# Optimization experiments

Hardware: AMD Instinct MI355X
Metric: run time of the kernel (lower is better)

## Reference

```python
import jax, jax.numpy as jnp
import numpy as np

B, H, L, D = 8, 8, 2048, 512

def setup_inputs() -> dict:
    key = jax.random.key(0)
    k1, k2 = jax.random.split(key)
    x = jax.random.normal(k1, (B, H, L, D), dtype=jnp.float32)
    mask = jnp.ones((B, L), dtype=jnp.int32)  # unused by the layer's call()
    complex_weight = 0.02 * jax.random.normal(k2, (H, L, D, 2), dtype=jnp.float32)
    return {"x": x, "mask": mask, "complex_weight": complex_weight}

def reference(x, mask, complex_weight):
    # FFT over the innermost (model_size) axis, matching tf.signal.fft
    fft_x = jnp.fft.fft(x.astype(jnp.complex64), axis=-1)
    w = jax.lax.complex(complex_weight[..., 0], complex_weight[..., 1])  # (H, L, D)
    gated = w * fft_x  # broadcast over batch
    out = jnp.fft.ifft(gated, axis=-1).real.astype(jnp.float32)
    return out
```

## Files before the change

kernel.cpp:

```cpp
#include <hip/hip_runtime.h>
#include <math.h>


#define HL 16384

__device__ __forceinline__ float2 cadd(float2 a, float2 b){ return make_float2(a.x+b.x, a.y+b.y); }
__device__ __forceinline__ float2 csub(float2 a, float2 b){ return make_float2(a.x-b.x, a.y-b.y); }
__device__ __forceinline__ float2 cmul(float2 a, float2 b){ return make_float2(a.x*b.x - a.y*b.y, a.x*b.y + a.y*b.x); }

__device__ __forceinline__ float2 twiddle(float f) {
    return make_float2(__builtin_amdgcn_cosf(f), -__builtin_amdgcn_sinf(f));
}

__device__ __forceinline__ void lds_order() {
    __builtin_amdgcn_wave_barrier();
}

__device__ __forceinline__ void fft8(float2 x[8]) {
    const float c = 0.70710678118654752f;
    float2 u0 = cadd(x[0], x[4]);
    float2 u1 = cadd(x[1], x[5]);
    float2 u2 = cadd(x[2], x[6]);
    float2 u3 = cadd(x[3], x[7]);
    float2 v0 = csub(x[0], x[4]);
    float2 t1 = csub(x[1], x[5]);
    float2 t2 = csub(x[2], x[6]);
    float2 t3 = csub(x[3], x[7]);
    float2 v1 = make_float2(c*(t1.x + t1.y), c*(t1.y - t1.x));
    float2 v2 = make_float2(t2.y, -t2.x);
    float2 v3 = make_float2(c*(t3.y - t3.x), -c*(t3.x + t3.y));
    float2 p0 = cadd(u0, u2), p1 = cadd(u1, u3);
    float2 q0 = csub(u0, u2), q1t = csub(u1, u3);
    float2 q1 = make_float2(q1t.y, -q1t.x);
    x[0] = cadd(p0, p1);
    x[4] = csub(p0, p1);
    x[2] = cadd(q0, q1);
    x[6] = csub(q0, q1);
    float2 r0 = cadd(v0, v2), r1 = cadd(v1, v3);
    float2 s0 = csub(v0, v2), s1t = csub(v1, v3);
    float2 s1 = make_float2(s1t.y, -s1t.x);
    x[1] = cadd(r0, r1);
    x[5] = csub(r0, r1);
    x[3] = cadd(s0, s1);
    x[7] = csub(s0, s1);
}

__device__ __forceinline__ void fft512_t(float2 v[8], int role, int lane, float2* sc,
                                         const float2* __restrict__ twA,
                                         const float2 tw2[8])
{
    fft8(v);
    #pragma unroll
    for (int k = 1; k < 8; ++k) v[k] = cmul(v[k], twA[role*7 + (k-1)]);
    lds_order();
    #pragma unroll
    for (int k1 = 0; k1 < 8; ++k1) sc[k1*72 + role] = v[k1];
    lds_order();
    const int k1 = lane >> 3, m2 = lane & 7;
    float2 u[8];
    #pragma unroll
    for (int m1 = 0; m1 < 8; ++m1) u[m1] = sc[k1*72 + 8*m1 + m2];
    fft8(u);
    #pragma unroll
    for (int j = 1; j < 8; ++j) u[j] = cmul(u[j], tw2[j]);
    lds_order();
    #pragma unroll
    for (int j1 = 0; j1 < 8; ++j1) sc[k1*72 + 9*j1 + m2] = u[j1];
    lds_order();
    const int j1 = lane & 7;
    #pragma unroll
    for (int m = 0; m < 8; ++m) v[m] = sc[k1*72 + 9*j1 + m];
    fft8(v);
}

using gu32 = __attribute__((address_space(1))) const unsigned int;
using lu32 = __attribute__((address_space(3))) unsigned int;

__global__ __launch_bounds__(256, 4) void sgn_fft_vec(
    const float* __restrict__ x,
    const float* __restrict__ cw,
    float* __restrict__ out)
{
    __shared__ __align__(16) float2 sc[4][8*72];
    __shared__ __align__(16) float  cwb[4][1024];
    __shared__ __align__(16) float2 twA[64*7];

    const int tid  = threadIdx.x;
    const int wid  = tid >> 6;
    const int lane = tid & 63;
    const int dsl  = ((lane & 7) << 3) | (lane >> 3);
    const int hl   = blockIdx.x;

    const int r1 = (wid       * HL + hl) * 512;
    const int r2 = ((wid + 4) * HL + hl) * 512;

    {
        const float* cwrow = cw + (size_t)hl * 1024;
        #pragma unroll
        for (int c = 0; c < 4; ++c) {
            __builtin_amdgcn_global_load_lds((gu32*)(cwrow + c*256 + lane*4),
                                             (lu32*)(&cwb[wid][c*256]), 16, 0, 0);
        }
    }

    const float4 a0 = *(const float4*)(x + r1 + 4*lane);
    const float4 a1 = *(const float4*)(x + r1 + 4*lane + 256);
    const float4 b0 = *(const float4*)(x + r2 + 4*lane);
    const float4 b1 = *(const float4*)(x + r2 + 4*lane + 256);

    {
        const int role = tid & 63, j = tid >> 6;
        twA[role*7 + 2*j] = twiddle((float)(role*(2*j+1)) * (1.0f/512.0f));
        if (j < 3)
            twA[role*7 + 2*j + 1] = twiddle((float)(role*(2*j+2)) * (1.0f/512.0f));
    }
    float2 tw2[8];
    {
        const int m2 = lane & 7;
        tw2[1] = twiddle((float)m2 * (1.0f/64.0f));
        tw2[2] = cmul(tw2[1], tw2[1]);
        tw2[3] = cmul(tw2[1], tw2[2]);
        tw2[4] = cmul(tw2[2], tw2[2]);
        tw2[5] = cmul(tw2[1], tw2[4]);
        tw2[6] = cmul(tw2[2], tw2[4]);
        tw2[7] = cmul(tw2[3], tw2[4]);
    }
    __syncthreads();

    float2* scw = &sc[wid][0];

    {
        float2* AB = scw;
        *(float4*)&AB[      4*lane    ] = make_float4(a0.x, b0.x, a0.y, b0.y);
        *(float4*)&AB[      4*lane + 2] = make_float4(a0.z, b0.z, a0.w, b0.w);
        *(float4*)&AB[256 + 4*lane    ] = make_float4(a1.x, b1.x, a1.y, b1.y);
        *(float4*)&AB[256 + 4*lane + 2] = make_float4(a1.z, b1.z, a1.w, b1.w);
    }
    lds_order();
    float2 v[8];
    #pragma unroll
    for (int j = 0; j < 8; ++j) v[j] = scw[64*j + lane];
    lds_order();

    fft512_t(v, lane, lane, scw, twA, tw2);

    asm volatile("s_waitcnt vmcnt(0)" ::: "memory");
    {
        const float2* __restrict__ cwf = (const float2*)&cwb[wid][0];
        const float hs = 0.5f / 512.0f;
        #pragma unroll
        for (int j2 = 0; j2 < 8; ++j2) {
            const int k  = dsl + 64*j2;
            const int nk = (512 - k) & 511;
            const float2 wk  = cwf[k];
            const float2 wnk = cwf[nk];
            const float2 wp  = make_float2(hs*(wk.x + wnk.x), hs*(wk.y - wnk.y));
            const float2 g   = cmul(wp, v[j2]);
            v[j2] = make_float2(g.x, -g.y);
        }
    }

    fft512_t(v, dsl, lane, scw, twA, tw2);

    lds_order();
    {
        float2* OD = scw;
        #pragma unroll
        for (int j2 = 0; j2 < 8; ++j2)
            OD[dsl + 64*j2] = make_float2(v[j2].x, -v[j2].y);
    }
    lds_order();
    #pragma unroll
    for (int c = 0; c < 2; ++c) {
        const float2* OD = scw;
        const float4 p = *(const float4*)&OD[4*lane + 256*c];
        const float4 q = *(const float4*)&OD[4*lane + 256*c + 2];
        *(float4*)(out + r1 + 4*lane + 256*c) = make_float4(p.x, p.z, q.x, q.z);
        *(float4*)(out + r2 + 4*lane + 256*c) = make_float4(p.y, p.w, q.y, q.w);
    }
}

extern "C" void kernel_launch(void* const* d_in, const int* in_sizes, int n_in,
                              void* d_out, int out_size, void* d_ws, size_t ws_size,
                              hipStream_t stream) {
    const float* x  = (const float*)d_in[0];
    const float* cw = (const float*)d_in[2];
    float* out = (float*)d_out;

    sgn_fft_vec<<<dim3(HL), dim3(256), 0, stream>>>(x, cw, out);
}
```

Baseline: 473.8 us.

## Load x via global_load_lds, weights into registers, compute twiddles per thread

Inputs x are now DMA'd straight into LDS with global_load_lds, replacing register loads followed by an LDS interleave store. Weights are gathered directly from global memory into registers rather than staged in LDS. The shared twiddle table is dropped in favour of per-thread twiddle generation, which removes the block-wide __syncthreads. The aim is less LDS traffic and no block barrier, at the cost of uncoalesced float2 weight gathers (each weight element is fetched twice, once as wk and once as wnk) and extra ALU work for the twiddles.

```diff
diff --git a/kernel.cpp b/kernel.cpp
--- a/kernel.cpp
+++ b/kernel.cpp
@@ -45,13 +45,26 @@
     x[7] = csub(s0, s1);
 }
 
-__device__ __forceinline__ void fft512_t(float2 v[8], int role, int lane, float2* sc,
-                                         const float2* __restrict__ twA,
+__device__ __forceinline__ void fft512_r(float2 v[8], int role, int lane, float2* sc,
                                          const float2 tw2[8])
 {
     fft8(v);
-    #pragma unroll
-    for (int k = 1; k < 8; ++k) v[k] = cmul(v[k], twA[role*7 + (k-1)]);
+    {
+        const float2 w1 = twiddle((float)role * (1.0f/512.0f));
+        const float2 w2 = cmul(w1, w1);
+        const float2 w3 = cmul(w1, w2);
+        const float2 w4 = cmul(w2, w2);
+        const float2 w5 = cmul(w1, w4);
+        const float2 w6 = cmul(w2, w4);
+        const float2 w7 = cmul(w3, w4);
+        v[1] = cmul(v[1], w1);
+        v[2] = cmul(v[2], w2);
+        v[3] = cmul(v[3], w3);
+        v[4] = cmul(v[4], w4);
+        v[5] = cmul(v[5], w5);
+        v[6] = cmul(v[6], w6);
+        v[7] = cmul(v[7], w7);
+    }
     lds_order();
     #pragma unroll
     for (int k1 = 0; k1 < 8; ++k1) sc[k1*72 + role] = v[k1];
@@ -76,14 +89,13 @@
 using gu32 = __attribute__((address_space(1))) const unsigned int;
 using lu32 = __attribute__((address_space(3))) unsigned int;
 
-__global__ __launch_bounds__(256, 4) void sgn_fft_vec(
+__global__ __launch_bounds__(256, 4) void sgn_fft_diet(
     const float* __restrict__ x,
     const float* __restrict__ cw,
     float* __restrict__ out)
 {
     __shared__ __align__(16) float2 sc[4][8*72];
-    __shared__ __align__(16) float  cwb[4][1024];
-    __shared__ __align__(16) float2 twA[64*7];
+    __shared__ __align__(16) float  xb[4][2][512];
 
     const int tid  = threadIdx.x;
     const int wid  = tid >> 6;
@@ -94,26 +106,15 @@
     const int r1 = (wid       * HL + hl) * 512;
     const int r2 = ((wid + 4) * HL + hl) * 512;
 
-    {
-        const float* cwrow = cw + (size_t)hl * 1024;
-        #pragma unroll
-        for (int c = 0; c < 4; ++c) {
-            __builtin_amdgcn_global_load_lds((gu32*)(cwrow + c*256 + lane*4),
-                                             (lu32*)(&cwb[wid][c*256]), 16, 0, 0);
-        }
+    #pragma unroll
+    for (int c = 0; c < 2; ++c) {
+        __builtin_amdgcn_global_load_lds((gu32*)(x + r1 + c*256 + 4*lane),
+                                         (lu32*)(&xb[wid][0][c*256]), 16, 0, 0);
+        __builtin_amdgcn_global_load_lds((gu32*)(x + r2 + c*256 + 4*lane),
+                                         (lu32*)(&xb[wid][1][c*256]), 16, 0, 0);
     }
+    __builtin_amdgcn_sched_barrier(0);
 
-    const float4 a0 = *(const float4*)(x + r1 + 4*lane);
-    const float4 a1 = *(const float4*)(x + r1 + 4*lane + 256);
-    const float4 b0 = *(const float4*)(x + r2 + 4*lane);
-    const float4 b1 = *(const float4*)(x + r2 + 4*lane + 256);
-
-    {
-        const int role = tid & 63, j = tid >> 6;
-        twA[role*7 + 2*j] = twiddle((float)(role*(2*j+1)) * (1.0f/512.0f));
-        if (j < 3)
-            twA[role*7 + 2*j + 1] = twiddle((float)(role*(2*j+2)) * (1.0f/512.0f));
-    }
     float2 tw2[8];
     {
         const int m2 = lane & 7;
@@ -125,42 +126,42 @@
         tw2[6] = cmul(tw2[2], tw2[4]);
         tw2[7] = cmul(tw2[3], tw2[4]);
     }
-    __syncthreads();
+
+    const float2* __restrict__ cw2 = (const float2*)cw;
+    const int wrow = hl * 512;
+    float2 wk[8], wnk[8];
+    #pragma unroll
+    for (int j2 = 0; j2 < 8; ++j2) {
+        const int k  = dsl + 64*j2;
+        const int nk = (512 - k) & 511;
+        wk[j2]  = cw2[wrow + k];
+        wnk[j2] = cw2[wrow + nk];
+    }
+
+    asm volatile("s_waitcnt vmcnt(16)" ::: "memory");
+
+    float2 v[8];
+    #pragma unroll
+    for (int j = 0; j < 8; ++j) {
+        v[j].x = xb[wid][0][64*j + lane];
+        v[j].y = xb[wid][1][64*j + lane];
+    }
 
     float2* scw = &sc[wid][0];
+    fft512_r(v, lane, lane, scw, tw2);
 
     {
-        float2* AB = scw;
-        *(float4*)&AB[      4*lane    ] = make_float4(a0.x, b0.x, a0.y, b0.y);
-        *(float4*)&AB[      4*lane + 2] = make_float4(a0.z, b0.z, a0.w, b0.w);
-        *(float4*)&AB[256 + 4*lane    ] = make_float4(a1.x, b1.x, a1.y, b1.y);
-        *(float4*)&AB[256 + 4*lane + 2] = make_float4(a1.z, b1.z, a1.w, b1.w);
-    }
-    lds_order();
-    float2 v[8];
-    #pragma unroll
-    for (int j = 0; j < 8; ++j) v[j] = scw[64*j + lane];
-    lds_order();
-
-    fft512_t(v, lane, lane, scw, twA, tw2);
-
-    asm volatile("s_waitcnt vmcnt(0)" ::: "memory");
-    {
-        const float2* __restrict__ cwf = (const float2*)&cwb[wid][0];
         const float hs = 0.5f / 512.0f;
         #pragma unroll
         for (int j2 = 0; j2 < 8; ++j2) {
-            const int k  = dsl + 64*j2;
-            const int nk = (512 - k) & 511;
-            const float2 wk  = cwf[k];
-            const float2 wnk = cwf[nk];
-            const float2 wp  = make_float2(hs*(wk.x + wnk.x), hs*(wk.y - wnk.y));
-            const float2 g   = cmul(wp, v[j2]);
+            const float2 wp = make_float2(hs*(wk[j2].x + wnk[j2].x),
+                                          hs*(wk[j2].y - wnk[j2].y));
+            const float2 g  = cmul(wp, v[j2]);
             v[j2] = make_float2(g.x, -g.y);
         }
     }
 
-    fft512_t(v, dsl, lane, scw, twA, tw2);
+    fft512_r(v, dsl, lane, scw, tw2);
 
     lds_order();
     {
@@ -187,5 +188,5 @@
     const float* cw = (const float*)d_in[2];
     float* out = (float*)d_out;
 
-    sgn_fft_vec<<<dim3(HL), dim3(256), 0, stream>>>(x, cw, out);
+    sgn_fft_diet<<<dim3(HL), dim3(256), 0, stream>>>(x, cw, out);
 }
```

Measured after the change: 477.4 us. Within noise of the previous version (+0.8%).
